# Optimization experiments

Measured on AMD Instinct MI355X. Metric: run time of the kernel, lower is better.

## Reference

```python
import jax, jax.numpy as jnp
import numpy as np

N_NODES = 50000
N_EDGES = 800000
HIDDEN = 128
N_LAYERS = 3
MAX_Z = 1000
N_GRAPHS = 512
LN_EPS = 1e-5


def setup_inputs() -> dict:
    key = jax.random.key(0)
    ks = jax.random.split(key, 16)
    s = 0.05
    inp = {
        "z": jax.random.randint(ks[0], (N_NODES,), 0, MAX_Z),
        "edge_index": jax.random.randint(ks[1], (2, N_EDGES), 0, N_NODES),
        "batch": jnp.sort(jax.random.randint(ks[2], (N_NODES,), 0, N_GRAPHS)),
        "z_table": jax.random.normal(ks[3], (MAX_Z, HIDDEN), jnp.float32) * s,
        "W1": jax.random.normal(ks[4], (N_LAYERS, HIDDEN, HIDDEN), jnp.float32) * s,
        "b1": jnp.zeros((N_LAYERS, HIDDEN), jnp.float32),
        "W2": jax.random.normal(ks[5], (N_LAYERS, HIDDEN, HIDDEN), jnp.float32) * s,
        "b2": jnp.zeros((N_LAYERS, HIDDEN), jnp.float32),
        "ln_g": jnp.ones((N_LAYERS, HIDDEN), jnp.float32),
        "ln_b": jnp.zeros((N_LAYERS, HIDDEN), jnp.float32),
        "lin1_W": jax.random.normal(ks[6], (N_LAYERS * HIDDEN, HIDDEN), jnp.float32) * s,
        "lin1_b": jnp.zeros((HIDDEN,), jnp.float32),
        "lin2_W": jax.random.normal(ks[7], (HIDDEN, 1), jnp.float32) * s,
        "lin2_b": jnp.zeros((1,), jnp.float32),
    }
    return inp


def _layernorm(h, g, b):
    mu = jnp.mean(h, axis=-1, keepdims=True)
    var = jnp.mean((h - mu) ** 2, axis=-1, keepdims=True)
    return g * (h - mu) * jax.lax.rsqrt(var + LN_EPS) + b


def _gin_conv(x, src, dst, W1, b1, W2, b2, g, b):
    # sum-aggregate neighbor features, eps = 0 (train_eps=False)
    agg = jax.ops.segment_sum(x[src], dst, num_segments=N_NODES)
    h = x + agg
    h = jax.nn.relu(h @ W1 + b1)
    h = jax.nn.relu(h @ W2 + b2)
    return _layernorm(h, g, b)


def reference(z, edge_index, batch, z_table, W1, b1, W2, b2, ln_g, ln_b,
              lin1_W, lin1_b, lin2_W, lin2_b):
    src, dst = edge_index[0], edge_index[1]
    x = z_table[z]  # [N, H] z embedding (z is 1-D so no sum over dim 1)
    xs = []
    for l in range(N_LAYERS):
        x = _gin_conv(x, src, dst, W1[l], b1[l], W2[l], b2[l], ln_g[l], ln_b[l])
        xs.append(x)
    xcat = jnp.concatenate(xs, axis=1)  # JK concat [N, L*H]
    # global mean pool over graphs
    sums = jax.ops.segment_sum(xcat, batch, num_segments=N_GRAPHS)
    cnts = jax.ops.segment_sum(jnp.ones((N_NODES, 1), xcat.dtype), batch,
                               num_segments=N_GRAPHS)
    pooled = sums / jnp.maximum(cnts, 1.0)
    h = jax.nn.relu(pooled @ lin1_W + lin1_b)
    # dropout is identity in eval mode
    return h @ lin2_W + lin2_b  # [N_GRAPHS, 1]
```

## Files before the change

kernel.cpp:

```cpp
#include <hip/hip_runtime.h>
#include <hip/hip_bf16.h>

#define NN 50000
#define NE 800000
#define HD 128
#define NL 3
#define NG 512
#define LN_EPS 1e-5f

typedef unsigned short u16;
typedef unsigned int u32;
typedef __attribute__((ext_vector_type(8))) short short8;
typedef __attribute__((ext_vector_type(4))) float f32x4;

__device__ __forceinline__ u16 f2bf(float f){
  u32 x = __float_as_uint(f);
  u32 r = (x + 0x7fffu + ((x >> 16) & 1u)) >> 16;
  return (u16)r;
}
__device__ __forceinline__ float blo(u32 u){ return __uint_as_float(u << 16); }
__device__ __forceinline__ float bhi(u32 u){ return __uint_as_float(u & 0xffff0000u); }
__device__ __forceinline__ u32 pk2(float a, float b){ return (u32)f2bf(a) | ((u32)f2bf(b) << 16); }

__device__ __forceinline__ int lower_bound_dev(const int* a, int n, int v){
  int lo = 0, hi = n;
  while (lo < hi){ int m = (lo + hi) >> 1; if (a[m] < v) lo = m + 1; else hi = m; }
  return lo;
}

__global__ __launch_bounds__(256) void k_prep_w(const float* __restrict__ W1,
    const float* __restrict__ W2, u16* __restrict__ Wt){
  int t = blockIdx.x * 256 + threadIdx.x;
  if (t >= 6 * 128 * 128) return;
  int w = t >> 14, r = t & 16383, n = r >> 7, k = r & 127;
  int l = w >> 1;
  const float* Ws = (w & 1) ? (W2 + l * 16384) : (W1 + l * 16384);
  Wt[t] = f2bf(Ws[k * 128 + n]);
}

__global__ __launch_bounds__(256) void k_embed(const int* __restrict__ z,
    const float* __restrict__ tab, u16* __restrict__ xb){
  int gt = blockIdx.x * 256 + threadIdx.x;
  int node = gt >> 5, q = gt & 31;
  float4 v = *reinterpret_cast<const float4*>(tab + (size_t)z[node] * 128 + q * 4);
  uint2 p = { pk2(v.x, v.y), pk2(v.z, v.w) };
  *reinterpret_cast<uint2*>(xb + (size_t)node * 128 + q * 4) = p;
}

__global__ __launch_bounds__(256) void k_count(const int* __restrict__ dst,
    int* __restrict__ deg){
  int e = blockIdx.x * 256 + threadIdx.x;
  if (e < NE) atomicAdd(&deg[dst[e]], 1);
}

__global__ __launch_bounds__(256) void k_scan1(const int* __restrict__ deg,
    int* __restrict__ part, int* __restrict__ bsum){
  int i = blockIdx.x * 256 + threadIdx.x;
  int v = (i < NN) ? deg[i] : 0;
  int lane = threadIdx.x & 63, wave = threadIdx.x >> 6;
  int s = v;
  for (int off = 1; off < 64; off <<= 1){ int n = __shfl_up(s, off); if (lane >= off) s += n; }
  __shared__ int wsums[4];
  if (lane == 63) wsums[wave] = s;
  __syncthreads();
  int add = 0;
  for (int w = 0; w < wave; ++w) add += wsums[w];
  int incl = s + add;
  if (i < NN) part[i] = incl - v;
  if (threadIdx.x == 255) bsum[blockIdx.x] = incl;
}

__global__ __launch_bounds__(256) void k_scan2(int* __restrict__ bsum, int nb){
  int tid = threadIdx.x;
  int v = (tid < nb) ? bsum[tid] : 0;
  int lane = tid & 63, wave = tid >> 6;
  int s = v;
  for (int off = 1; off < 64; off <<= 1){ int n = __shfl_up(s, off); if (lane >= off) s += n; }
  __shared__ int wsums[4];
  if (lane == 63) wsums[wave] = s;
  __syncthreads();
  int add = 0;
  for (int w = 0; w < wave; ++w) add += wsums[w];
  int incl = s + add;
  if (tid < nb) bsum[tid] = incl - v;
}

__global__ __launch_bounds__(256) void k_scan3(const int* __restrict__ part,
    const int* __restrict__ bsum, int* __restrict__ rowptr, int* __restrict__ cursor){
  int i = blockIdx.x * 256 + threadIdx.x;
  if (i < NN){ int r = part[i] + bsum[blockIdx.x]; rowptr[i] = r; cursor[i] = r; }
  if (i == 0) rowptr[NN] = NE;
}

__global__ __launch_bounds__(256) void k_fill(const int* __restrict__ src,
    const int* __restrict__ dst, int* __restrict__ cursor, int* __restrict__ col){
  int e = blockIdx.x * 256 + threadIdx.x;
  if (e < NE){ int p = atomicAdd(&cursor[dst[e]], 1); col[p] = src[e]; }
}

__global__ __launch_bounds__(256) void k_gather(const int* __restrict__ rowptr,
    const int* __restrict__ col, const u16* __restrict__ xb, u16* __restrict__ hb){
  int wave = threadIdx.x >> 6, lane = threadIdx.x & 63;
  int node = blockIdx.x * 4 + wave;
  int half = lane >> 5, l5 = lane & 31;
  float a0 = 0.f, a1 = 0.f, a2 = 0.f, a3 = 0.f;
  if (half == 0){
    uint2 s = *reinterpret_cast<const uint2*>(xb + (size_t)node * 128 + l5 * 4);
    a0 = blo(s.x); a1 = bhi(s.x); a2 = blo(s.y); a3 = bhi(s.y);
  }
  int lo = rowptr[node], hi = rowptr[node + 1];
  for (int e = lo + half; e < hi; e += 2){
    int c = col[e];
    uint2 v = *reinterpret_cast<const uint2*>(xb + (size_t)c * 128 + l5 * 4);
    a0 += blo(v.x); a1 += bhi(v.x); a2 += blo(v.y); a3 += bhi(v.y);
  }
  a0 += __shfl_xor(a0, 32); a1 += __shfl_xor(a1, 32);
  a2 += __shfl_xor(a2, 32); a3 += __shfl_xor(a3, 32);
  if (half == 0){
    uint2 p = { pk2(a0, a1), pk2(a2, a3) };
    *reinterpret_cast<uint2*>(hb + (size_t)node * 128 + l5 * 4) = p;
  }
}

template<int DO_LN>
__global__ __launch_bounds__(256) void k_gemm_f(const u16* __restrict__ A,
    const u16* __restrict__ Wt, const float* __restrict__ bias,
    const float* __restrict__ lng, const float* __restrict__ lnb,
    u16* __restrict__ Cout){
  __shared__ u16 As[128 * 128];
  __shared__ u16 Bs[128 * 128];
  int tid = threadIdx.x;
  int rb = blockIdx.x * 128;

  #pragma unroll
  for (int i = 0; i < 8; ++i){
    int u = tid + i * 256;
    int n = u >> 4, k8 = u & 15;
    uint4 w = *reinterpret_cast<const uint4*>(Wt + n * 128 + k8 * 8);
    *reinterpret_cast<uint4*>(&Bs[n * 128 + (k8 ^ (n & 15)) * 8]) = w;
  }
  #pragma unroll
  for (int i = 0; i < 8; ++i){
    int u = tid + i * 256;
    int row = u >> 4, k8 = u & 15;
    int grow = rb + row;
    uint4 v = {0u, 0u, 0u, 0u};
    if (grow < NN) v = *reinterpret_cast<const uint4*>(A + (size_t)grow * 128 + k8 * 8);
    *reinterpret_cast<uint4*>(&As[row * 128 + (k8 ^ (row & 15)) * 8]) = v;
  }
  __syncthreads();

  int wave = tid >> 6, lane = tid & 63;
  int lrow = lane & 15, kgrp = lane >> 4;
  f32x4 acc[2][8];
  #pragma unroll
  for (int rt = 0; rt < 2; ++rt)
    #pragma unroll
    for (int nt = 0; nt < 8; ++nt) acc[rt][nt] = (f32x4){0.f, 0.f, 0.f, 0.f};

  #pragma unroll
  for (int ks = 0; ks < 4; ++ks){
    int ch = ks * 4 + kgrp;
    short8 a0 = *reinterpret_cast<const short8*>(&As[(wave * 32 + lrow) * 128 + (ch ^ lrow) * 8]);
    short8 a1 = *reinterpret_cast<const short8*>(&As[(wave * 32 + 16 + lrow) * 128 + (ch ^ lrow) * 8]);
    #pragma unroll
    for (int nt = 0; nt < 8; ++nt){
      short8 b = *reinterpret_cast<const short8*>(&Bs[(nt * 16 + lrow) * 128 + (ch ^ lrow) * 8]);
      acc[0][nt] = __builtin_amdgcn_mfma_f32_16x16x32_bf16(a0, b, acc[0][nt], 0, 0, 0);
      acc[1][nt] = __builtin_amdgcn_mfma_f32_16x16x32_bf16(a1, b, acc[1][nt], 0, 0, 0);
    }
  }

  float bv[8], gv[8], lbv[8];
  #pragma unroll
  for (int nt = 0; nt < 8; ++nt){
    int gcol = nt * 16 + lrow;
    bv[nt] = __ldg(bias + gcol);
    if (DO_LN){ gv[nt] = __ldg(lng + gcol); lbv[nt] = __ldg(lnb + gcol); }
  }
  #pragma unroll
  for (int rt = 0; rt < 2; ++rt)
    #pragma unroll
    for (int nt = 0; nt < 8; ++nt)
      #pragma unroll
      for (int j = 0; j < 4; ++j)
        acc[rt][nt][j] = fmaxf(acc[rt][nt][j] + bv[nt], 0.f);

  if (DO_LN){
    #pragma unroll
    for (int rt = 0; rt < 2; ++rt)
      #pragma unroll
      for (int j = 0; j < 4; ++j){
        float s = 0.f, sq = 0.f;
        #pragma unroll
        for (int nt = 0; nt < 8; ++nt){ float v = acc[rt][nt][j]; s += v; sq += v * v; }
        #pragma unroll
        for (int off = 1; off < 16; off <<= 1){
          s += __shfl_xor(s, off); sq += __shfl_xor(sq, off);
        }
        float mu = s * (1.f / 128.f);
        float var = sq * (1.f / 128.f) - mu * mu;
        float rstd = rsqrtf(var + LN_EPS);
        #pragma unroll
        for (int nt = 0; nt < 8; ++nt)
          acc[rt][nt][j] = gv[nt] * (acc[rt][nt][j] - mu) * rstd + lbv[nt];
      }
  }

  #pragma unroll
  for (int rt = 0; rt < 2; ++rt){
    int rbase = rb + wave * 32 + rt * 16 + kgrp * 4;
    #pragma unroll
    for (int nt = 0; nt < 8; ++nt){
      int gcol = nt * 16 + lrow;
      #pragma unroll
      for (int j = 0; j < 4; ++j){
        int grow = rbase + j;
        if (grow < NN) Cout[(size_t)grow * 128 + gcol] = f2bf(acc[rt][nt][j]);
      }
    }
  }
}

__global__ __launch_bounds__(256) void k_pool(const u16* __restrict__ xb,
    const int* __restrict__ batch, float* __restrict__ pooled, int lslice){
  int g = blockIdx.x;
  int w = threadIdx.x >> 6, lane = threadIdx.x & 63;
  __shared__ float red[4][128];
  int lo = lower_bound_dev(batch, NN, g);
  int hi = lower_bound_dev(batch, NN, g + 1);
  float s0 = 0.f, s1 = 0.f;
  for (int i = lo + w; i < hi; i += 4){
    u32 u = *reinterpret_cast<const u32*>(xb + (size_t)i * 128 + lane * 2);
    s0 += blo(u); s1 += bhi(u);
  }
  red[w][lane * 2] = s0; red[w][lane * 2 + 1] = s1;
  __syncthreads();
  int f = threadIdx.x;
  if (f < 128)
    pooled[(size_t)g * 384 + lslice * 128 + f] = red[0][f] + red[1][f] + red[2][f] + red[3][f];
}

__global__ __launch_bounds__(128) void k_final(const float* __restrict__ pooled,
    const int* __restrict__ batch, const float* __restrict__ W1,
    const float* __restrict__ b1, const float* __restrict__ W2,
    const float* __restrict__ b2, float* __restrict__ out){
  int g = blockIdx.x, f = threadIdx.x;
  int lo = lower_bound_dev(batch, NN, g);
  int hi = lower_bound_dev(batch, NN, g + 1);
  float scale = 1.f / fmaxf((float)(hi - lo), 1.f);
  __shared__ float p[384];
  for (int k = f; k < 384; k += 128) p[k] = pooled[(size_t)g * 384 + k] * scale;
  __syncthreads();
  float acc = __ldg(b1 + f);
  for (int k = 0; k < 384; ++k) acc += p[k] * __ldg(W1 + k * 128 + f);
  float hval = fmaxf(acc, 0.f);
  float v = hval * __ldg(W2 + f);
  for (int off = 32; off; off >>= 1) v += __shfl_xor(v, off);
  __shared__ float red[2];
  int lane = f & 63, wave = f >> 6;
  if (lane == 0) red[wave] = v;
  __syncthreads();
  if (f == 0) out[g] = red[0] + red[1] + __ldg(b2);
}

extern "C" void kernel_launch(void* const* d_in, const int* in_sizes, int n_in,
                              void* d_out, int out_size, void* d_ws, size_t ws_size,
                              hipStream_t stream){
  const int*   z     = (const int*)d_in[0];
  const int*   ei    = (const int*)d_in[1];
  const int*   batch = (const int*)d_in[2];
  const float* ztab  = (const float*)d_in[3];
  const float* W1    = (const float*)d_in[4];
  const float* b1    = (const float*)d_in[5];
  const float* W2    = (const float*)d_in[6];
  const float* b2    = (const float*)d_in[7];
  const float* lng   = (const float*)d_in[8];
  const float* lnb   = (const float*)d_in[9];
  const float* l1W   = (const float*)d_in[10];
  const float* l1b   = (const float*)d_in[11];
  const float* l2W   = (const float*)d_in[12];
  const float* l2b   = (const float*)d_in[13];
  float* out = (float*)d_out;

  char* wsb = (char*)d_ws;
  size_t off = 0;
  auto alloc = [&](size_t bytes){ void* p = wsb + off; off += (bytes + 255) & ~(size_t)255; return p; };
  u16*   xbf    = (u16*)alloc((size_t)NN * 128 * 2);
  u16*   hbf    = (u16*)alloc((size_t)NN * 128 * 2);
  u16*   h1bf   = (u16*)alloc((size_t)NN * 128 * 2);
  float* pooled = (float*)alloc((size_t)NG * 384 * 4);
  u16*   Wt     = (u16*)alloc((size_t)6 * 128 * 128 * 2);
  int*   deg    = (int*)alloc((size_t)NN * 4);
  int*   part   = (int*)alloc((size_t)NN * 4);
  int*   bsum   = (int*)alloc((size_t)256 * 4);
  int*   rowptr = (int*)alloc((size_t)(NN + 1) * 4);
  int*   cursor = (int*)alloc((size_t)NN * 4);
  int*   col    = (int*)alloc((size_t)NE * 4);

  const int* srcv = ei;
  const int* dstv = ei + NE;

  hipMemsetAsync(deg, 0, (size_t)NN * 4, stream);
  k_prep_w<<<(6 * 128 * 128 + 255) / 256, 256, 0, stream>>>(W1, W2, Wt);
  k_embed<<<NN * 32 / 256, 256, 0, stream>>>(z, ztab, xbf);
  k_count<<<(NE + 255) / 256, 256, 0, stream>>>(dstv, deg);
  int nb = (NN + 255) / 256;
  k_scan1<<<nb, 256, 0, stream>>>(deg, part, bsum);
  k_scan2<<<1, 256, 0, stream>>>(bsum, nb);
  k_scan3<<<nb, 256, 0, stream>>>(part, bsum, rowptr, cursor);
  k_fill<<<(NE + 255) / 256, 256, 0, stream>>>(srcv, dstv, cursor, col);

  int gb = (NN + 127) / 128;
  for (int l = 0; l < NL; ++l){
    k_gather<<<NN / 4, 256, 0, stream>>>(rowptr, col, xbf, hbf);
    k_gemm_f<0><<<gb, 256, 0, stream>>>(hbf,  Wt + (size_t)(l * 2 + 0) * 16384,
                                        b1 + l * 128, nullptr, nullptr, h1bf);
    k_gemm_f<1><<<gb, 256, 0, stream>>>(h1bf, Wt + (size_t)(l * 2 + 1) * 16384,
                                        b2 + l * 128, lng + l * 128, lnb + l * 128, xbf);
    k_pool<<<NG, 256, 0, stream>>>(xbf, batch, pooled, l);
  }
  k_final<<<NG, 128, 0, stream>>>(pooled, batch, l1W, l1b, l2W, l2b, out);
}
```

Measured before the change: 467.8 us.

## Fuse both GIN MLP GEMMs into one kernel and widen gather loads

The two per-layer GEMM kernels become one: the first GEMM's ReLU output is written back to shared memory as bf16, and the second weight matrix, prefetched into registers beforehand, is then stored into the same LDS buffer. This removes the h1 intermediate's global write and read and one launch per layer. The gather kernel now has each quarter-wave load 16-byte vectors, processing two edges per iteration with separate accumulators, and reduces across quarters with shuffles. The cost is higher register pressure from holding the prefetched weights and more syncs inside the fused kernel.

Result: faster. 424.5 us (-9.3%).

```diff
diff --git a/kernel.cpp b/kernel.cpp
--- a/kernel.cpp
+++ b/kernel.cpp
@@ -102,33 +102,50 @@
     const int* __restrict__ col, const u16* __restrict__ xb, u16* __restrict__ hb){
   int wave = threadIdx.x >> 6, lane = threadIdx.x & 63;
   int node = blockIdx.x * 4 + wave;
-  int half = lane >> 5, l5 = lane & 31;
-  float a0 = 0.f, a1 = 0.f, a2 = 0.f, a3 = 0.f;
-  if (half == 0){
-    uint2 s = *reinterpret_cast<const uint2*>(xb + (size_t)node * 128 + l5 * 4);
-    a0 = blo(s.x); a1 = bhi(s.x); a2 = blo(s.y); a3 = bhi(s.y);
+  int q = lane >> 4, l4 = lane & 15;
+  float a[8] = {0.f,0.f,0.f,0.f,0.f,0.f,0.f,0.f};
+  float b[8] = {0.f,0.f,0.f,0.f,0.f,0.f,0.f,0.f};
+  if (q == 0){
+    uint4 s = *reinterpret_cast<const uint4*>(xb + (size_t)node * 128 + l4 * 8);
+    a[0] = blo(s.x); a[1] = bhi(s.x); a[2] = blo(s.y); a[3] = bhi(s.y);
+    a[4] = blo(s.z); a[5] = bhi(s.z); a[6] = blo(s.w); a[7] = bhi(s.w);
   }
   int lo = rowptr[node], hi = rowptr[node + 1];
-  for (int e = lo + half; e < hi; e += 2){
-    int c = col[e];
-    uint2 v = *reinterpret_cast<const uint2*>(xb + (size_t)c * 128 + l5 * 4);
-    a0 += blo(v.x); a1 += bhi(v.x); a2 += blo(v.y); a3 += bhi(v.y);
-  }
-  a0 += __shfl_xor(a0, 32); a1 += __shfl_xor(a1, 32);
-  a2 += __shfl_xor(a2, 32); a3 += __shfl_xor(a3, 32);
-  if (half == 0){
-    uint2 p = { pk2(a0, a1), pk2(a2, a3) };
-    *reinterpret_cast<uint2*>(hb + (size_t)node * 128 + l5 * 4) = p;
-  }
-}
-
-template<int DO_LN>
-__global__ __launch_bounds__(256) void k_gemm_f(const u16* __restrict__ A,
-    const u16* __restrict__ Wt, const float* __restrict__ bias,
+  int e = lo + q;
+  for (; e + 4 < hi; e += 8){
+    int c0 = col[e], c1 = col[e + 4];
+    uint4 v0 = *reinterpret_cast<const uint4*>(xb + (size_t)c0 * 128 + l4 * 8);
+    uint4 v1 = *reinterpret_cast<const uint4*>(xb + (size_t)c1 * 128 + l4 * 8);
+    a[0] += blo(v0.x); a[1] += bhi(v0.x); a[2] += blo(v0.y); a[3] += bhi(v0.y);
+    a[4] += blo(v0.z); a[5] += bhi(v0.z); a[6] += blo(v0.w); a[7] += bhi(v0.w);
+    b[0] += blo(v1.x); b[1] += bhi(v1.x); b[2] += blo(v1.y); b[3] += bhi(v1.y);
+    b[4] += blo(v1.z); b[5] += bhi(v1.z); b[6] += blo(v1.w); b[7] += bhi(v1.w);
+  }
+  if (e < hi){
+    int c0 = col[e];
+    uint4 v0 = *reinterpret_cast<const uint4*>(xb + (size_t)c0 * 128 + l4 * 8);
+    a[0] += blo(v0.x); a[1] += bhi(v0.x); a[2] += blo(v0.y); a[3] += bhi(v0.y);
+    a[4] += blo(v0.z); a[5] += bhi(v0.z); a[6] += blo(v0.w); a[7] += bhi(v0.w);
+  }
+  #pragma unroll
+  for (int j = 0; j < 8; ++j){
+    a[j] += b[j];
+    a[j] += __shfl_xor(a[j], 16);
+    a[j] += __shfl_xor(a[j], 32);
+  }
+  if (q == 0){
+    uint4 p = { pk2(a[0], a[1]), pk2(a[2], a[3]), pk2(a[4], a[5]), pk2(a[6], a[7]) };
+    *reinterpret_cast<uint4*>(hb + (size_t)node * 128 + l4 * 8) = p;
+  }
+}
+
+__global__ __launch_bounds__(256) void k_layer(const u16* __restrict__ A,
+    const u16* __restrict__ Wt1, const u16* __restrict__ Wt2,
+    const float* __restrict__ bias1, const float* __restrict__ bias2,
     const float* __restrict__ lng, const float* __restrict__ lnb,
     u16* __restrict__ Cout){
   __shared__ u16 As[128 * 128];
-  __shared__ u16 Bs[128 * 128];
+  __shared__ u16 Ws[128 * 128];
   int tid = threadIdx.x;
   int rb = blockIdx.x * 128;
 
@@ -136,8 +153,8 @@
   for (int i = 0; i < 8; ++i){
     int u = tid + i * 256;
     int n = u >> 4, k8 = u & 15;
-    uint4 w = *reinterpret_cast<const uint4*>(Wt + n * 128 + k8 * 8);
-    *reinterpret_cast<uint4*>(&Bs[n * 128 + (k8 ^ (n & 15)) * 8]) = w;
+    uint4 w = *reinterpret_cast<const uint4*>(Wt1 + n * 128 + k8 * 8);
+    *reinterpret_cast<uint4*>(&Ws[n * 128 + (k8 ^ (n & 15)) * 8]) = w;
   }
   #pragma unroll
   for (int i = 0; i < 8; ++i){
@@ -150,6 +167,14 @@
   }
   __syncthreads();
 
+  uint4 w2r[8];
+  #pragma unroll
+  for (int i = 0; i < 8; ++i){
+    int u = tid + i * 256;
+    int n = u >> 4, k8 = u & 15;
+    w2r[i] = *reinterpret_cast<const uint4*>(Wt2 + n * 128 + k8 * 8);
+  }
+
   int wave = tid >> 6, lane = tid & 63;
   int lrow = lane & 15, kgrp = lane >> 4;
   f32x4 acc[2][8];
@@ -165,47 +190,92 @@
     short8 a1 = *reinterpret_cast<const short8*>(&As[(wave * 32 + 16 + lrow) * 128 + (ch ^ lrow) * 8]);
     #pragma unroll
     for (int nt = 0; nt < 8; ++nt){
-      short8 b = *reinterpret_cast<const short8*>(&Bs[(nt * 16 + lrow) * 128 + (ch ^ lrow) * 8]);
+      short8 b = *reinterpret_cast<const short8*>(&Ws[(nt * 16 + lrow) * 128 + (ch ^ lrow) * 8]);
       acc[0][nt] = __builtin_amdgcn_mfma_f32_16x16x32_bf16(a0, b, acc[0][nt], 0, 0, 0);
       acc[1][nt] = __builtin_amdgcn_mfma_f32_16x16x32_bf16(a1, b, acc[1][nt], 0, 0, 0);
     }
   }
 
-  float bv[8], gv[8], lbv[8];
+  #pragma unroll
+  for (int nt = 0; nt < 8; ++nt){
+    float bv = __ldg(bias1 + nt * 16 + lrow);
+    #pragma unroll
+    for (int rt = 0; rt < 2; ++rt)
+      #pragma unroll
+      for (int j = 0; j < 4; ++j)
+        acc[rt][nt][j] = fmaxf(acc[rt][nt][j] + bv, 0.f);
+  }
+
+  __syncthreads();
+
+  #pragma unroll
+  for (int i = 0; i < 8; ++i){
+    int u = tid + i * 256;
+    int n = u >> 4, k8 = u & 15;
+    *reinterpret_cast<uint4*>(&Ws[n * 128 + (k8 ^ (n & 15)) * 8]) = w2r[i];
+  }
+  #pragma unroll
+  for (int rt = 0; rt < 2; ++rt)
+    #pragma unroll
+    for (int j = 0; j < 4; ++j){
+      int row = wave * 32 + rt * 16 + kgrp * 4 + j;
+      #pragma unroll
+      for (int nt = 0; nt < 8; ++nt){
+        int col = nt * 16 + lrow;
+        int ch = (col >> 3) ^ (row & 15);
+        As[row * 128 + ch * 8 + (col & 7)] = f2bf(acc[rt][nt][j]);
+      }
+    }
+  __syncthreads();
+
+  #pragma unroll
+  for (int rt = 0; rt < 2; ++rt)
+    #pragma unroll
+    for (int nt = 0; nt < 8; ++nt) acc[rt][nt] = (f32x4){0.f, 0.f, 0.f, 0.f};
+
+  #pragma unroll
+  for (int ks = 0; ks < 4; ++ks){
+    int ch = ks * 4 + kgrp;
+    short8 a0 = *reinterpret_cast<const short8*>(&As[(wave * 32 + lrow) * 128 + (ch ^ lrow) * 8]);
+    short8 a1 = *reinterpret_cast<const short8*>(&As[(wave * 32 + 16 + lrow) * 128 + (ch ^ lrow) * 8]);
+    #pragma unroll
+    for (int nt = 0; nt < 8; ++nt){
+      short8 b = *reinterpret_cast<const short8*>(&Ws[(nt * 16 + lrow) * 128 + (ch ^ lrow) * 8]);
+      acc[0][nt] = __builtin_amdgcn_mfma_f32_16x16x32_bf16(a0, b, acc[0][nt], 0, 0, 0);
+      acc[1][nt] = __builtin_amdgcn_mfma_f32_16x16x32_bf16(a1, b, acc[1][nt], 0, 0, 0);
+    }
+  }
+
+  float gv[8], lbv[8];
   #pragma unroll
   for (int nt = 0; nt < 8; ++nt){
     int gcol = nt * 16 + lrow;
-    bv[nt] = __ldg(bias + gcol);
-    if (DO_LN){ gv[nt] = __ldg(lng + gcol); lbv[nt] = __ldg(lnb + gcol); }
+    float bv = __ldg(bias2 + gcol);
+    gv[nt] = __ldg(lng + gcol); lbv[nt] = __ldg(lnb + gcol);
+    #pragma unroll
+    for (int rt = 0; rt < 2; ++rt)
+      #pragma unroll
+      for (int j = 0; j < 4; ++j)
+        acc[rt][nt][j] = fmaxf(acc[rt][nt][j] + bv, 0.f);
   }
   #pragma unroll
   for (int rt = 0; rt < 2; ++rt)
     #pragma unroll
-    for (int nt = 0; nt < 8; ++nt)
-      #pragma unroll
-      for (int j = 0; j < 4; ++j)
-        acc[rt][nt][j] = fmaxf(acc[rt][nt][j] + bv[nt], 0.f);
-
-  if (DO_LN){
-    #pragma unroll
-    for (int rt = 0; rt < 2; ++rt)
-      #pragma unroll
-      for (int j = 0; j < 4; ++j){
-        float s = 0.f, sq = 0.f;
-        #pragma unroll
-        for (int nt = 0; nt < 8; ++nt){ float v = acc[rt][nt][j]; s += v; sq += v * v; }
-        #pragma unroll
-        for (int off = 1; off < 16; off <<= 1){
-          s += __shfl_xor(s, off); sq += __shfl_xor(sq, off);
-        }
-        float mu = s * (1.f / 128.f);
-        float var = sq * (1.f / 128.f) - mu * mu;
-        float rstd = rsqrtf(var + LN_EPS);
-        #pragma unroll
-        for (int nt = 0; nt < 8; ++nt)
-          acc[rt][nt][j] = gv[nt] * (acc[rt][nt][j] - mu) * rstd + lbv[nt];
+    for (int j = 0; j < 4; ++j){
+      float s = 0.f, sq = 0.f;
+      #pragma unroll
+      for (int nt = 0; nt < 8; ++nt){ float v = acc[rt][nt][j]; s += v; sq += v * v; }
+      #pragma unroll
+      for (int off = 1; off < 16; off <<= 1){
+        s += __shfl_xor(s, off); sq += __shfl_xor(sq, off);
       }
-  }
+      float mu = s * (1.f / 128.f);
+      float var = sq * (1.f / 128.f) - mu * mu;
+      float rstd = rsqrtf(var + LN_EPS);
+      #pragma unroll
+      for (int nt = 0; nt < 8; ++nt)
+        acc[rt][nt][j] = gv[nt] * (acc[rt][nt][j] - mu) * rstd + lbv[nt];
+    }
 
   #pragma unroll
   for (int rt = 0; rt < 2; ++rt){
@@ -288,7 +358,6 @@
   auto alloc = [&](size_t bytes){ void* p = wsb + off; off += (bytes + 255) & ~(size_t)255; return p; };
   u16*   xbf    = (u16*)alloc((size_t)NN * 128 * 2);
   u16*   hbf    = (u16*)alloc((size_t)NN * 128 * 2);
-  u16*   h1bf   = (u16*)alloc((size_t)NN * 128 * 2);
   float* pooled = (float*)alloc((size_t)NG * 384 * 4);
   u16*   Wt     = (u16*)alloc((size_t)6 * 128 * 128 * 2);
   int*   deg    = (int*)alloc((size_t)NN * 4);
@@ -314,10 +383,9 @@
   int gb = (NN + 127) / 128;
   for (int l = 0; l < NL; ++l){
     k_gather<<<NN / 4, 256, 0, stream>>>(rowptr, col, xbf, hbf);
-    k_gemm_f<0><<<gb, 256, 0, stream>>>(hbf,  Wt + (size_t)(l * 2 + 0) * 16384,
-                                        b1 + l * 128, nullptr, nullptr, h1bf);
-    k_gemm_f<1><<<gb, 256, 0, stream>>>(h1bf, Wt + (size_t)(l * 2 + 1) * 16384,
-                                        b2 + l * 128, lng + l * 128, lnb + l * 128, xbf);
+    k_layer<<<gb, 256, 0, stream>>>(hbf,
+        Wt + (size_t)(l * 2 + 0) * 16384, Wt + (size_t)(l * 2 + 1) * 16384,
+        b1 + l * 128, b2 + l * 128, lng + l * 128, lnb + l * 128, xbf);
     k_pool<<<NG, 256, 0, stream>>>(xbf, batch, pooled, l);
   }
   k_final<<<NG, 128, 0, stream>>>(pooled, batch, l1W, l1b, l2W, l2b, out);
```
